# Performance work log

Hardware: AMD Instinct MI355X
Metric: run time of the kernel (lower is better)

## Reference

```python
import jax, jax.numpy as jnp
import numpy as np

MAX_LEN = 256
EMBED_DIM = 256
SEQ_LEN = 256
BATCH = 2048
NUM_PEAKS = 8


def setup_inputs() -> dict:
    key = jax.random.key(0)
    k1, k2, k3 = jax.random.split(key, 3)
    x = jax.random.normal(k1, (SEQ_LEN, BATCH, EMBED_DIM), dtype=jnp.float32)
    # some positions >= SEQ_LEN are invalid and must be masked out
    peak_positions = jax.random.randint(k2, (BATCH, NUM_PEAKS), 0, 300, dtype=jnp.int64)
    table = jax.random.normal(k3, (MAX_LEN, EMBED_DIM), dtype=jnp.float32)  # nn.Embedding weight
    return {"x": x, "peak_positions": peak_positions, "table": table}


def _sinusoidal_pe(seq_len, dim, dtype):
    # NB: original uses log(1000.0), not 10000.0 -- kept faithful.
    position = jnp.arange(seq_len, dtype=jnp.float32)[:, None]            # [S, 1]
    div_term = jnp.exp(jnp.arange(0, dim, 2, dtype=jnp.float32) * (-np.log(1000.0) / dim))
    ang = position * div_term                                              # [S, D/2]
    pe = jnp.zeros((seq_len, dim), dtype=jnp.float32)
    pe = pe.at[:, 0::2].set(jnp.sin(ang)).at[:, 1::2].set(jnp.cos(ang))
    return pe.astype(dtype)


def reference(x, peak_positions, table):
    seq_len, batch, dim = x.shape
    max_len = table.shape[0]
    # positional encoding add
    pe = _sinusoidal_pe(seq_len, dim, x.dtype)                             # [S, D]
    x = x + pe[:, None, :]
    # batched masked gather-scatter (replaces the per-sample Python loop)
    valid = (peak_positions >= 0) & (peak_positions < seq_len)             # [B, P]
    # route invalid peaks to a dump row (seq_len) that is sliced off after scatter
    idx = jnp.where(valid, peak_positions, seq_len)                        # [B, P]
    emb = table[jnp.clip(peak_positions, 0, max_len - 1)]                  # [B, P, D]
    b_idx = jnp.arange(batch)[:, None]                                     # [B, 1]
    peak_embed = (
        jnp.zeros((seq_len + 1, batch, dim), dtype=x.dtype)
        .at[idx, b_idx].set(emb)[:seq_len]                                 # [S, B, D]
    )
    return x + peak_embed
```

## Files before the change

### kernel.cpp

```cpp
#include <hip/hip_runtime.h>


namespace {
constexpr int S      = 256;
constexpr int Bn     = 2048;
constexpr int D      = 256;
constexpr int P      = 8;
constexpr int D4     = D / 4;
constexpr int BTILE  = 128;
constexpr int NBT    = Bn / BTILE;
constexpr int THREADS = 256;
constexpr int ITERS  = BTILE * D4 / THREADS;
}

__global__ __launch_bounds__(THREADS)
void pe_peak_kernel(const float* __restrict__ x,
                    const unsigned* __restrict__ pk,
                    const float* __restrict__ table,
                    float* __restrict__ out)
{
    __shared__ float4 s_pe[D4];
    __shared__ float4 s_pt[D4];
    __shared__ unsigned char s_mask[BTILE];
    __shared__ int s_is64;

    const int t  = threadIdx.x;
    const int s  = blockIdx.x >> 4;
    const int b0 = (blockIdx.x & (NBT - 1)) * BTILE;

    if (t == 0) {
        unsigned o = 0;
        #pragma unroll
        for (int i = 0; i < 32; ++i) o |= pk[2 * i + 1];
        s_is64 = (o == 0) ? 1 : 0;
    }

    if (t < D4) {
        const float c = -6.907755278982137f / 256.0f;
        float a0 = (float)s * expf((float)(4 * t) * c);
        float a1 = (float)s * expf((float)(4 * t + 2) * c);
        float4 pe4 = make_float4(sinf(a0), cosf(a0), sinf(a1), cosf(a1));
        float4 tb4 = reinterpret_cast<const float4*>(table)[s * D4 + t];
        s_pe[t] = pe4;
        s_pt[t] = make_float4(pe4.x + tb4.x, pe4.y + tb4.y,
                              pe4.z + tb4.z, pe4.w + tb4.w);
    }
    __syncthreads();

    if (t < BTILE) {
        const int b = b0 + t;
        unsigned m = 0;
        if (s_is64) {
            #pragma unroll
            for (int p = 0; p < P; ++p) m |= (pk[(size_t)(b * P + p) * 2] == (unsigned)s);
        } else {
            #pragma unroll
            for (int p = 0; p < P; ++p) m |= (pk[b * P + p] == (unsigned)s);
        }
        s_mask[t] = (unsigned char)m;
    }
    __syncthreads();

    const size_t base = ((size_t)s * Bn + b0) * D4;
    const float4* __restrict__ xr = reinterpret_cast<const float4*>(x) + base;
    float4* __restrict__ orow     = reinterpret_cast<float4*>(out) + base;

    #pragma unroll 8
    for (int j = 0; j < ITERS; ++j) {
        const int i  = j * THREADS + t;
        const float4* __restrict__ addsrc = s_mask[i >> 6] ? s_pt : s_pe;
        const float4 a = addsrc[i & 63];
        float4 v = xr[i];
        v.x += a.x; v.y += a.y; v.z += a.z; v.w += a.w;
        orow[i] = v;
    }
}

extern "C" void kernel_launch(void* const* d_in, const int* in_sizes, int n_in,
                              void* d_out, int out_size, void* d_ws, size_t ws_size,
                              hipStream_t stream) {
    const float*    x     = (const float*)d_in[0];
    const unsigned* pk    = (const unsigned*)d_in[1];
    const float*    table = (const float*)d_in[2];
    float*          out   = (float*)d_out;

    pe_peak_kernel<<<dim3(S * NBT), dim3(THREADS), 0, stream>>>(x, pk, table, out);
}
```

Measured before the change: 217.3 us.

## Flatten to grid-stride kernel with rotated sinusoid recurrence and nontemporal access

Replaces the per-(s, batch-tile) block scheme with a persistent grid where each thread owns a (batch, d4) position and walks over sequence rows. Positional encodings are advanced with a sin/cos rotation recurrence instead of shared-memory tables and block syncs. Peak masks become per-wave 64-bit bitmasks. Loads and stores of x/out use nontemporal hints. This removes shared memory and barriers but risks accumulating recurrence error.

Result: no change. 217.1 us (-0.1%).

```diff
diff --git a/kernel.cpp b/kernel.cpp
--- a/kernel.cpp
+++ b/kernel.cpp
@@ -1,78 +1,83 @@
 #include <hip/hip_runtime.h>
 
 
+typedef float f32x4 __attribute__((ext_vector_type(4)));
+
 namespace {
-constexpr int S      = 256;
-constexpr int Bn     = 2048;
-constexpr int D      = 256;
-constexpr int P      = 8;
-constexpr int D4     = D / 4;
-constexpr int BTILE  = 128;
-constexpr int NBT    = Bn / BTILE;
+constexpr int S       = 256;
+constexpr int Bn      = 2048;
+constexpr int P       = 8;
+constexpr int D4      = 64;
 constexpr int THREADS = 256;
-constexpr int ITERS  = BTILE * D4 / THREADS;
+constexpr int BLOCKS  = 2048;
+constexpr int GSTRIDE = BLOCKS * THREADS;
+constexpr int KITER   = (S * Bn * D4) / GSTRIDE;
 }
 
 __global__ __launch_bounds__(THREADS)
-void pe_peak_kernel(const float* __restrict__ x,
-                    const unsigned* __restrict__ pk,
-                    const float* __restrict__ table,
-                    float* __restrict__ out)
+void pe_peak_flat(const float* __restrict__ x,
+                  const unsigned* __restrict__ pk,
+                  const float* __restrict__ table,
+                  float* __restrict__ out)
 {
-    __shared__ float4 s_pe[D4];
-    __shared__ float4 s_pt[D4];
-    __shared__ unsigned char s_mask[BTILE];
-    __shared__ int s_is64;
+    const int t  = threadIdx.x;
+    const int g  = blockIdx.x * THREADS + t;
+    const int d4 = g & 63;
+    const int b  = (g >> 6) & (Bn - 1);
+    const int s0 = g >> 17;
 
-    const int t  = threadIdx.x;
-    const int s  = blockIdx.x >> 4;
-    const int b0 = (blockIdx.x & (NBT - 1)) * BTILE;
+    const unsigned hw = pk[2 * (t & 63) + 1];
+    const bool is64 = (__ballot(hw != 0u) == 0ull);
 
-    if (t == 0) {
-        unsigned o = 0;
+    unsigned long long hm = 0;
+    if (is64) {
         #pragma unroll
-        for (int i = 0; i < 32; ++i) o |= pk[2 * i + 1];
-        s_is64 = (o == 0) ? 1 : 0;
+        for (int p = 0; p < P; ++p) {
+            unsigned v = pk[(size_t)(b * P + p) * 2];
+            if (v < (unsigned)S && (v & 3u) == (unsigned)s0) hm |= 1ull << (v >> 2);
+        }
+    } else {
+        #pragma unroll
+        for (int p = 0; p < P; ++p) {
+            unsigned v = pk[b * P + p];
+            if (v < (unsigned)S && (v & 3u) == (unsigned)s0) hm |= 1ull << (v >> 2);
+        }
     }
+    const unsigned hmlo = __builtin_amdgcn_readfirstlane((unsigned)hm);
+    const unsigned hmhi = __builtin_amdgcn_readfirstlane((unsigned)(hm >> 32));
+    const unsigned long long hmu = ((unsigned long long)hmhi << 32) | hmlo;
 
-    if (t < D4) {
-        const float c = -6.907755278982137f / 256.0f;
-        float a0 = (float)s * expf((float)(4 * t) * c);
-        float a1 = (float)s * expf((float)(4 * t + 2) * c);
-        float4 pe4 = make_float4(sinf(a0), cosf(a0), sinf(a1), cosf(a1));
-        float4 tb4 = reinterpret_cast<const float4*>(table)[s * D4 + t];
-        s_pe[t] = pe4;
-        s_pt[t] = make_float4(pe4.x + tb4.x, pe4.y + tb4.y,
-                              pe4.z + tb4.z, pe4.w + tb4.w);
-    }
-    __syncthreads();
+    const float c  = -6.907755278982137f / 256.0f;
+    const float f0 = expf((float)(4 * d4) * c);
+    const float f1 = expf((float)(4 * d4 + 2) * c);
+    float sa = sinf((float)s0 * f0), ca = cosf((float)s0 * f0);
+    float sb = sinf((float)s0 * f1), cb = cosf((float)s0 * f1);
+    const float r0c = cosf(4.0f * f0), r0s = sinf(4.0f * f0);
+    const float r1c = cosf(4.0f * f1), r1s = sinf(4.0f * f1);
 
-    if (t < BTILE) {
-        const int b = b0 + t;
-        unsigned m = 0;
-        if (s_is64) {
-            #pragma unroll
-            for (int p = 0; p < P; ++p) m |= (pk[(size_t)(b * P + p) * 2] == (unsigned)s);
-        } else {
-            #pragma unroll
-            for (int p = 0; p < P; ++p) m |= (pk[b * P + p] == (unsigned)s);
-        }
-        s_mask[t] = (unsigned char)m;
-    }
-    __syncthreads();
+    const f32x4* __restrict__ xr = reinterpret_cast<const f32x4*>(x);
+    f32x4* __restrict__ ow       = reinterpret_cast<f32x4*>(out);
+    const f32x4* __restrict__ tr = reinterpret_cast<const f32x4*>(table);
 
-    const size_t base = ((size_t)s * Bn + b0) * D4;
-    const float4* __restrict__ xr = reinterpret_cast<const float4*>(x) + base;
-    float4* __restrict__ orow     = reinterpret_cast<float4*>(out) + base;
+    size_t off  = (size_t)g;
+    int    tidx = s0 * D4 + d4;
 
     #pragma unroll 8
-    for (int j = 0; j < ITERS; ++j) {
-        const int i  = j * THREADS + t;
-        const float4* __restrict__ addsrc = s_mask[i >> 6] ? s_pt : s_pe;
-        const float4 a = addsrc[i & 63];
-        float4 v = xr[i];
-        v.x += a.x; v.y += a.y; v.z += a.z; v.w += a.w;
-        orow[i] = v;
+    for (int k = 0; k < KITER; ++k) {
+        f32x4 v = __builtin_nontemporal_load(xr + off);
+        f32x4 r;
+        r.x = v.x + sa; r.y = v.y + ca;
+        r.z = v.z + sb; r.w = v.w + cb;
+        if ((hmu >> k) & 1ull) {
+            f32x4 tb = tr[tidx];
+            r += tb;
+        }
+        __builtin_nontemporal_store(r, ow + off);
+        float nsa = sa * r0c + ca * r0s, nca = ca * r0c - sa * r0s;
+        float nsb = sb * r1c + cb * r1s, ncb = cb * r1c - sb * r1s;
+        sa = nsa; ca = nca; sb = nsb; cb = ncb;
+        off  += (size_t)GSTRIDE;
+        tidx += 4 * D4;
     }
 }
 
@@ -84,5 +89,5 @@
     const float*    table = (const float*)d_in[2];
     float*          out   = (float*)d_out;
 
-    pe_peak_kernel<<<dim3(S * NBT), dim3(THREADS), 0, stream>>>(x, pk, table, out);
+    pe_peak_flat<<<dim3(BLOCKS), dim3(THREADS), 0, stream>>>(x, pk, table, out);
 }
```
